# Kernel optimization log

Measured on AMD Instinct MI355X. Metric: run time of the kernel, lower is better.

Reference implementation:

```python
import jax, jax.numpy as jnp
import numpy as np

EPS = 1e-6
B_PAIRS, N_PER_GRAPH, D_IN, D_OUT = 128, 64, 128, 128
N_NODES = B_PAIRS * N_PER_GRAPH          # 8192 nodes on each side
N_EDGES = B_PAIRS * N_PER_GRAPH * N_PER_GRAPH  # 524288 dense bipartite edges


def setup_inputs() -> dict:
    key = jax.random.key(0)
    k1, k2, k3 = jax.random.split(key, 3)
    x_src = jax.random.normal(k1, (N_NODES, D_IN), dtype=jnp.float32)
    x_tgt = jax.random.normal(k2, (N_NODES, D_IN), dtype=jnp.float32)
    # xavier-uniform-like weight [out_nhid, in_nhid]
    bound = np.sqrt(6.0 / (D_OUT + D_IN))
    weight = jax.random.uniform(k3, (D_OUT, D_IN), dtype=jnp.float32,
                                minval=-bound, maxval=bound)
    # block-diagonal dense bipartite edges: graph pair p connects its n x n nodes
    base = np.arange(B_PAIRS, dtype=np.int64)[:, None, None] * N_PER_GRAPH
    src = (base + np.arange(N_PER_GRAPH, dtype=np.int64)[:, None]).repeat(N_PER_GRAPH, axis=2)
    dst = (base + np.arange(N_PER_GRAPH, dtype=np.int64)[None, None, :]).repeat(N_PER_GRAPH, axis=1)
    edge_src = jnp.asarray(src.reshape(-1))
    edge_dst = jnp.asarray(dst.reshape(-1))
    return {"x_src": x_src, "x_tgt": x_tgt, "weight": weight,
            "edge_src": edge_src, "edge_dst": edge_dst}


def reference(x_src, x_tgt, weight, edge_src, edge_dst):
    M = x_tgt.shape[0]
    # --- message: per-edge relu(cosine similarity), softmax-like normalization per target ---
    x_j = x_src[edge_src]                      # [E, D] gather source features
    x_i = x_tgt[edge_dst]                      # [E, D] gather target features
    n_i = jnp.linalg.norm(x_i, axis=-1, keepdims=True)
    n_j = jnp.linalg.norm(x_j, axis=-1, keepdims=True)
    x_norm = jnp.maximum(n_i * n_j, EPS)
    coef = jax.nn.relu(jnp.sum(x_i * x_j, axis=1, keepdims=True) / x_norm)  # [E,1]
    coef_sum = jax.ops.segment_sum(coef + EPS, edge_dst, num_segments=M)    # [M,1]
    norm_coef = coef / coef_sum[edge_dst]
    global_x = jax.ops.segment_sum(norm_coef * x_j, edge_dst, num_segments=M)  # [M,D]
    # --- per-output-channel cosine between weight-scaled target and aggregated features ---
    # numerator[m,o] = sum_d x_tgt[m,d] * global_x[m,d] * weight[o,d]^2  (avoids [M,O,D] blowup)
    W2 = weight * weight                       # [O, D]
    numerator = (x_tgt * global_x) @ W2.T      # [M, O]
    den_t = jnp.sqrt((x_tgt * x_tgt) @ W2.T + EPS)
    den_g = jnp.sqrt((global_x * global_x) @ W2.T + EPS)
    denominator = jnp.maximum(den_t * den_g, EPS)
    return numerator / denominator             # [M, out_nhid]
```

## Files before the change

kernel.cpp:

```cpp
#include <hip/hip_runtime.h>

#define EPS 1e-6f

typedef __bf16 bf16_t;
typedef bf16_t bf16x8 __attribute__((ext_vector_type(8)));
typedef float  f32x4  __attribute__((ext_vector_type(4)));

namespace {
constexpr int D  = 128;
constexpr int OD = 128;
constexpr int SXS_S = 136;
constexpr int SCF_S = 72;
constexpr int SF_S  = 132;
}

__device__ inline bf16x8 to_bf16x8(float4 a, float4 b) {
    bf16x8 r;
    r[0] = (bf16_t)a.x; r[1] = (bf16_t)a.y; r[2] = (bf16_t)a.z; r[3] = (bf16_t)a.w;
    r[4] = (bf16_t)b.x; r[5] = (bf16_t)b.y; r[6] = (bf16_t)b.z; r[7] = (bf16_t)b.w;
    return r;
}

__global__ __launch_bounds__(512, 4)
void h2mn_fused(const float* __restrict__ x_src,
                const float* __restrict__ x_tgt,
                const float* __restrict__ weight,
                float* __restrict__ out)
{
    __shared__ __attribute__((aligned(16))) bf16_t sXs[64][SXS_S];
    __shared__ __attribute__((aligned(16))) bf16_t sCf[16][SCF_S];
    __shared__ __attribute__((aligned(16))) float  sXt[16][SF_S];
    __shared__ __attribute__((aligned(16))) float  sGx[16][SF_S];
    __shared__ float ns[64], ntg[16], csum[16];

    const int t = threadIdx.x;
    const int p = blockIdx.x >> 2;
    const int h = blockIdx.x & 3;

    {
        const float4* src = reinterpret_cast<const float4*>(x_src + (size_t)p * 64 * D);
        #pragma unroll
        for (int k = 0; k < 2; ++k) {
            const int c = t + 512 * k;
            const int j = c >> 4, d0 = (c & 15) * 8;
            const float4 v0 = src[c * 2], v1 = src[c * 2 + 1];
            float ss = v0.x*v0.x + v0.y*v0.y + v0.z*v0.z + v0.w*v0.w
                     + v1.x*v1.x + v1.y*v1.y + v1.z*v1.z + v1.w*v1.w;
            #pragma unroll
            for (int mk = 1; mk < 16; mk <<= 1) ss += __shfl_xor(ss, mk);
            if ((t & 15) == 0) ns[j] = sqrtf(ss);
            *reinterpret_cast<bf16x8*>(&sXs[j][d0]) = to_bf16x8(v0, v1);
        }
    }
    if (t < 256) {
        const float4* tg = reinterpret_cast<const float4*>(x_tgt + (size_t)(p * 64 + h * 16) * D);
        const int c = t;
        const int i = c >> 4, d0 = (c & 15) * 8;
        const float4 v0 = tg[c * 2], v1 = tg[c * 2 + 1];
        float ss = v0.x*v0.x + v0.y*v0.y + v0.z*v0.z + v0.w*v0.w
                 + v1.x*v1.x + v1.y*v1.y + v1.z*v1.z + v1.w*v1.w;
        #pragma unroll
        for (int mk = 1; mk < 16; mk <<= 1) ss += __shfl_xor(ss, mk);
        if ((t & 15) == 0) ntg[i] = sqrtf(ss);
        *reinterpret_cast<float4*>(&sXt[i][d0])     = v0;
        *reinterpret_cast<float4*>(&sXt[i][d0 + 4]) = v1;
    }
    __syncthreads();

    const int w  = t >> 6;
    const int ln = t & 63;
    const int mm = ln & 15;
    const int g  = ln >> 4;

    if (w < 4) {
        const int nt = w;
        f32x4 accS = {0.f, 0.f, 0.f, 0.f};
        #pragma unroll
        for (int ks = 0; ks < 4; ++ks) {
            const float* xp = &sXt[mm][ks * 32 + g * 8];
            const float4 x0 = *reinterpret_cast<const float4*>(xp);
            const float4 x1 = *reinterpret_cast<const float4*>(xp + 4);
            const bf16x8 a = to_bf16x8(x0, x1);
            const bf16x8 b = *reinterpret_cast<const bf16x8*>(&sXs[nt * 16 + mm][ks * 32 + g * 8]);
            accS = __builtin_amdgcn_mfma_f32_16x16x32_bf16(a, b, accS, 0, 0, 0);
        }
        const int j_loc = nt * 16 + mm;
        const float nsj = ns[j_loc];
        #pragma unroll
        for (int r = 0; r < 4; ++r) {
            const int m_loc = g * 4 + r;
            const float den = fmaxf(ntg[m_loc] * nsj, EPS);
            const float cf  = fmaxf(accS[r] / den, 0.f);
            sCf[m_loc][j_loc] = (bf16_t)cf;
        }
    }
    __syncthreads();

    if (t < 256) {
        const int row = t >> 4, c0 = (t & 15) * 4;
        float s = (float)sCf[row][c0]     + (float)sCf[row][c0 + 1]
                + (float)sCf[row][c0 + 2] + (float)sCf[row][c0 + 3];
        #pragma unroll
        for (int mk = 1; mk < 16; mk <<= 1) s += __shfl_xor(s, mk);
        if ((t & 15) == 0) csum[row] = s + 64.f * EPS;
    }
    __syncthreads();

    const float* wrow = weight + (size_t)(w * 16 + mm) * D + g * 8;
    float4 wr0[4], wr1[4];
    #pragma unroll
    for (int ks = 0; ks < 4; ++ks) {
        wr0[ks] = *reinterpret_cast<const float4*>(wrow + ks * 32);
        wr1[ks] = *reinterpret_cast<const float4*>(wrow + ks * 32 + 4);
    }

    {
        f32x4 accG = {0.f, 0.f, 0.f, 0.f};
        #pragma unroll
        for (int ks = 0; ks < 2; ++ks) {
            const bf16x8 a = *reinterpret_cast<const bf16x8*>(&sCf[mm][ks * 32 + g * 8]);
            bf16x8 b;
            #pragma unroll
            for (int i2 = 0; i2 < 8; ++i2)
                b[i2] = sXs[ks * 32 + g * 8 + i2][w * 16 + mm];
            accG = __builtin_amdgcn_mfma_f32_16x16x32_bf16(a, b, accG, 0, 0, 0);
        }
        float inv[4];
        #pragma unroll
        for (int r = 0; r < 4; ++r) inv[r] = 1.f / csum[g * 4 + r];
        #pragma unroll
        for (int r = 0; r < 4; ++r)
            sGx[g * 4 + r][w * 16 + mm] = accG[r] * inv[r];
    }
    __syncthreads();

    {
        f32x4 nume = {0.f,0.f,0.f,0.f};
        f32x4 det  = {0.f,0.f,0.f,0.f};
        f32x4 deg  = {0.f,0.f,0.f,0.f};
        #pragma unroll
        for (int ks = 0; ks < 4; ++ks) {
            const float* xp = &sXt[mm][ks * 32 + g * 8];
            const float* gp = &sGx[mm][ks * 32 + g * 8];
            const float4 x0 = *reinterpret_cast<const float4*>(xp);
            const float4 x1 = *reinterpret_cast<const float4*>(xp + 4);
            const float4 g0 = *reinterpret_cast<const float4*>(gp);
            const float4 g1 = *reinterpret_cast<const float4*>(gp + 4);
            const float xv[8] = {x0.x,x0.y,x0.z,x0.w,x1.x,x1.y,x1.z,x1.w};
            const float gv[8] = {g0.x,g0.y,g0.z,g0.w,g1.x,g1.y,g1.z,g1.w};
            bf16x8 af, bf_, cf_;
            #pragma unroll
            for (int i2 = 0; i2 < 8; ++i2) {
                af [i2] = (bf16_t)(xv[i2] * gv[i2]);
                bf_[i2] = (bf16_t)(xv[i2] * xv[i2]);
                cf_[i2] = (bf16_t)(gv[i2] * gv[i2]);
            }
            float4 w0 = wr0[ks], w1 = wr1[ks];
            w0.x *= w0.x; w0.y *= w0.y; w0.z *= w0.z; w0.w *= w0.w;
            w1.x *= w1.x; w1.y *= w1.y; w1.z *= w1.z; w1.w *= w1.w;
            const bf16x8 wv = to_bf16x8(w0, w1);
            nume = __builtin_amdgcn_mfma_f32_16x16x32_bf16(af,  wv, nume, 0, 0, 0);
            det  = __builtin_amdgcn_mfma_f32_16x16x32_bf16(bf_, wv, det,  0, 0, 0);
            deg  = __builtin_amdgcn_mfma_f32_16x16x32_bf16(cf_, wv, deg,  0, 0, 0);
        }
        const int o = w * 16 + mm;
        #pragma unroll
        for (int r = 0; r < 4; ++r) {
            const int m_loc = g * 4 + r;
            const int mg = p * 64 + h * 16 + m_loc;
            const float dd = fmaxf(sqrtf(det[r] + EPS) * sqrtf(deg[r] + EPS), EPS);
            out[(size_t)mg * OD + o] = nume[r] / dd;
        }
    }
}

extern "C" void kernel_launch(void* const* d_in, const int* in_sizes, int n_in,
                              void* d_out, int out_size, void* d_ws, size_t ws_size,
                              hipStream_t stream)
{
    const float* x_src  = (const float*)d_in[0];
    const float* x_tgt  = (const float*)d_in[1];
    const float* weight = (const float*)d_in[2];
    float* out = (float*)d_out;

    h2mn_fused<<<dim3(512), dim3(512), 0, stream>>>(x_src, x_tgt, weight, out);
}
```

Baseline: 73.91 us.

## Precompute bf16 MFMA operands in shared memory and overlap weight loads

Stores x_tgt in bf16 once in shared memory for the similarity MFMA. The squared and product operands for the final projection (x*g, x^2, g^2) are now computed cooperatively into shared bf16 tiles instead of redundantly by every wave. The x^2 tile is built by the idle waves 4-7 during the similarity stage. The weight load is moved ahead of the similarity stage and squared once into registers. This removes duplicated conversion work across the eight waves, at the cost of more shared memory (lower occupancy risk) and one extra barrier.

```diff
diff --git a/kernel.cpp b/kernel.cpp
--- a/kernel.cpp
+++ b/kernel.cpp
@@ -4,6 +4,7 @@
 
 typedef __bf16 bf16_t;
 typedef bf16_t bf16x8 __attribute__((ext_vector_type(8)));
+typedef bf16_t bf16x4 __attribute__((ext_vector_type(4)));
 typedef float  f32x4  __attribute__((ext_vector_type(4)));
 
 namespace {
@@ -12,6 +13,7 @@
 constexpr int SXS_S = 136;
 constexpr int SCF_S = 72;
 constexpr int SF_S  = 132;
+constexpr int SB_S  = 136;
 }
 
 __device__ inline bf16x8 to_bf16x8(float4 a, float4 b) {
@@ -27,10 +29,14 @@
                 const float* __restrict__ weight,
                 float* __restrict__ out)
 {
-    __shared__ __attribute__((aligned(16))) bf16_t sXs[64][SXS_S];
-    __shared__ __attribute__((aligned(16))) bf16_t sCf[16][SCF_S];
-    __shared__ __attribute__((aligned(16))) float  sXt[16][SF_S];
-    __shared__ __attribute__((aligned(16))) float  sGx[16][SF_S];
+    __shared__ __attribute__((aligned(16))) bf16_t sXs [64][SXS_S];
+    __shared__ __attribute__((aligned(16))) bf16_t sXtB[16][SB_S];
+    __shared__ __attribute__((aligned(16))) bf16_t sCf [16][SCF_S];
+    __shared__ __attribute__((aligned(16))) float  sXt [16][SF_S];
+    __shared__ __attribute__((aligned(16))) float  sGx [16][SF_S];
+    __shared__ __attribute__((aligned(16))) bf16_t sAf [16][SB_S];
+    __shared__ __attribute__((aligned(16))) bf16_t sBf [16][SB_S];
+    __shared__ __attribute__((aligned(16))) bf16_t sCg [16][SB_S];
     __shared__ float ns[64], ntg[16], csum[16];
 
     const int t = threadIdx.x;
@@ -64,6 +70,7 @@
         if ((t & 15) == 0) ntg[i] = sqrtf(ss);
         *reinterpret_cast<float4*>(&sXt[i][d0])     = v0;
         *reinterpret_cast<float4*>(&sXt[i][d0 + 4]) = v1;
+        *reinterpret_cast<bf16x8*>(&sXtB[i][d0])    = to_bf16x8(v0, v1);
     }
     __syncthreads();
 
@@ -71,40 +78,6 @@
     const int ln = t & 63;
     const int mm = ln & 15;
     const int g  = ln >> 4;
-
-    if (w < 4) {
-        const int nt = w;
-        f32x4 accS = {0.f, 0.f, 0.f, 0.f};
-        #pragma unroll
-        for (int ks = 0; ks < 4; ++ks) {
-            const float* xp = &sXt[mm][ks * 32 + g * 8];
-            const float4 x0 = *reinterpret_cast<const float4*>(xp);
-            const float4 x1 = *reinterpret_cast<const float4*>(xp + 4);
-            const bf16x8 a = to_bf16x8(x0, x1);
-            const bf16x8 b = *reinterpret_cast<const bf16x8*>(&sXs[nt * 16 + mm][ks * 32 + g * 8]);
-            accS = __builtin_amdgcn_mfma_f32_16x16x32_bf16(a, b, accS, 0, 0, 0);
-        }
-        const int j_loc = nt * 16 + mm;
-        const float nsj = ns[j_loc];
-        #pragma unroll
-        for (int r = 0; r < 4; ++r) {
-            const int m_loc = g * 4 + r;
-            const float den = fmaxf(ntg[m_loc] * nsj, EPS);
-            const float cf  = fmaxf(accS[r] / den, 0.f);
-            sCf[m_loc][j_loc] = (bf16_t)cf;
-        }
-    }
-    __syncthreads();
-
-    if (t < 256) {
-        const int row = t >> 4, c0 = (t & 15) * 4;
-        float s = (float)sCf[row][c0]     + (float)sCf[row][c0 + 1]
-                + (float)sCf[row][c0 + 2] + (float)sCf[row][c0 + 3];
-        #pragma unroll
-        for (int mk = 1; mk < 16; mk <<= 1) s += __shfl_xor(s, mk);
-        if ((t & 15) == 0) csum[row] = s + 64.f * EPS;
-    }
-    __syncthreads();
 
     const float* wrow = weight + (size_t)(w * 16 + mm) * D + g * 8;
     float4 wr0[4], wr1[4];
@@ -112,6 +85,55 @@
     for (int ks = 0; ks < 4; ++ks) {
         wr0[ks] = *reinterpret_cast<const float4*>(wrow + ks * 32);
         wr1[ks] = *reinterpret_cast<const float4*>(wrow + ks * 32 + 4);
+    }
+
+    if (w < 4) {
+        const int nt = w;
+        f32x4 accS = {0.f, 0.f, 0.f, 0.f};
+        #pragma unroll
+        for (int ks = 0; ks < 4; ++ks) {
+            const bf16x8 a = *reinterpret_cast<const bf16x8*>(&sXtB[mm][ks * 32 + g * 8]);
+            const bf16x8 b = *reinterpret_cast<const bf16x8*>(&sXs[nt * 16 + mm][ks * 32 + g * 8]);
+            accS = __builtin_amdgcn_mfma_f32_16x16x32_bf16(a, b, accS, 0, 0, 0);
+        }
+        const int j_loc = nt * 16 + mm;
+        const float nsj = ns[j_loc];
+        #pragma unroll
+        for (int r = 0; r < 4; ++r) {
+            const int m_loc = g * 4 + r;
+            const float den = fmaxf(ntg[m_loc] * nsj, EPS);
+            const float cf  = fmaxf(accS[r] / den, 0.f);
+            sCf[m_loc][j_loc] = (bf16_t)cf;
+        }
+    } else {
+        const int u   = t - 256;
+        const int row = u >> 4, d0 = (u & 15) * 8;
+        const float4 x0 = *reinterpret_cast<const float4*>(&sXt[row][d0]);
+        const float4 x1 = *reinterpret_cast<const float4*>(&sXt[row][d0 + 4]);
+        float4 q0, q1;
+        q0.x = x0.x*x0.x; q0.y = x0.y*x0.y; q0.z = x0.z*x0.z; q0.w = x0.w*x0.w;
+        q1.x = x1.x*x1.x; q1.y = x1.y*x1.y; q1.z = x1.z*x1.z; q1.w = x1.w*x1.w;
+        *reinterpret_cast<bf16x8*>(&sBf[row][d0]) = to_bf16x8(q0, q1);
+    }
+    __syncthreads();
+
+    if (t < 256) {
+        const int row = t >> 4, c0 = (t & 15) * 4;
+        float s = (float)sCf[row][c0]     + (float)sCf[row][c0 + 1]
+                + (float)sCf[row][c0 + 2] + (float)sCf[row][c0 + 3];
+        #pragma unroll
+        for (int mk = 1; mk < 16; mk <<= 1) s += __shfl_xor(s, mk);
+        if ((t & 15) == 0) csum[row] = s + 64.f * EPS;
+    }
+    __syncthreads();
+
+    bf16x8 wq[4];
+    #pragma unroll
+    for (int ks = 0; ks < 4; ++ks) {
+        float4 w0 = wr0[ks], w1 = wr1[ks];
+        w0.x *= w0.x; w0.y *= w0.y; w0.z *= w0.z; w0.w *= w0.w;
+        w1.x *= w1.x; w1.y *= w1.y; w1.z *= w1.z; w1.w *= w1.w;
+        wq[ks] = to_bf16x8(w0, w1);
     }
 
     {
@@ -135,33 +157,32 @@
     __syncthreads();
 
     {
+        const int row = t >> 5, d0 = (t & 31) * 4;
+        const float4 xv = *reinterpret_cast<const float4*>(&sXt[row][d0]);
+        const float4 gv = *reinterpret_cast<const float4*>(&sGx[row][d0]);
+        bf16x4 a4, c4;
+        a4[0] = (bf16_t)(xv.x * gv.x); a4[1] = (bf16_t)(xv.y * gv.y);
+        a4[2] = (bf16_t)(xv.z * gv.z); a4[3] = (bf16_t)(xv.w * gv.w);
+        c4[0] = (bf16_t)(gv.x * gv.x); c4[1] = (bf16_t)(gv.y * gv.y);
+        c4[2] = (bf16_t)(gv.z * gv.z); c4[3] = (bf16_t)(gv.w * gv.w);
+        *reinterpret_cast<bf16x4*>(&sAf[row][d0]) = a4;
+        *reinterpret_cast<bf16x4*>(&sCg[row][d0]) = c4;
+    }
+    __syncthreads();
+
+    {
         f32x4 nume = {0.f,0.f,0.f,0.f};
         f32x4 det  = {0.f,0.f,0.f,0.f};
         f32x4 deg  = {0.f,0.f,0.f,0.f};
         #pragma unroll
         for (int ks = 0; ks < 4; ++ks) {
-            const float* xp = &sXt[mm][ks * 32 + g * 8];
-            const float* gp = &sGx[mm][ks * 32 + g * 8];
-            const float4 x0 = *reinterpret_cast<const float4*>(xp);
-            const float4 x1 = *reinterpret_cast<const float4*>(xp + 4);
-            const float4 g0 = *reinterpret_cast<const float4*>(gp);
-            const float4 g1 = *reinterpret_cast<const float4*>(gp + 4);
-            const float xv[8] = {x0.x,x0.y,x0.z,x0.w,x1.x,x1.y,x1.z,x1.w};
-            const float gv[8] = {g0.x,g0.y,g0.z,g0.w,g1.x,g1.y,g1.z,g1.w};
-            bf16x8 af, bf_, cf_;
-            #pragma unroll
-            for (int i2 = 0; i2 < 8; ++i2) {
-                af [i2] = (bf16_t)(xv[i2] * gv[i2]);
-                bf_[i2] = (bf16_t)(xv[i2] * xv[i2]);
-                cf_[i2] = (bf16_t)(gv[i2] * gv[i2]);
-            }
-            float4 w0 = wr0[ks], w1 = wr1[ks];
-            w0.x *= w0.x; w0.y *= w0.y; w0.z *= w0.z; w0.w *= w0.w;
-            w1.x *= w1.x; w1.y *= w1.y; w1.z *= w1.z; w1.w *= w1.w;
-            const bf16x8 wv = to_bf16x8(w0, w1);
-            nume = __builtin_amdgcn_mfma_f32_16x16x32_bf16(af,  wv, nume, 0, 0, 0);
-            det  = __builtin_amdgcn_mfma_f32_16x16x32_bf16(bf_, wv, det,  0, 0, 0);
-            deg  = __builtin_amdgcn_mfma_f32_16x16x32_bf16(cf_, wv, deg,  0, 0, 0);
+            const int k0 = ks * 32 + g * 8;
+            const bf16x8 af  = *reinterpret_cast<const bf16x8*>(&sAf[mm][k0]);
+            const bf16x8 bf_ = *reinterpret_cast<const bf16x8*>(&sBf[mm][k0]);
+            const bf16x8 cf_ = *reinterpret_cast<const bf16x8*>(&sCg[mm][k0]);
+            nume = __builtin_amdgcn_mfma_f32_16x16x32_bf16(af,  wq[ks], nume, 0, 0, 0);
+            det  = __builtin_amdgcn_mfma_f32_16x16x32_bf16(bf_, wq[ks], det,  0, 0, 0);
+            deg  = __builtin_amdgcn_mfma_f32_16x16x32_bf16(cf_, wq[ks], deg,  0, 0, 0);
         }
         const int o = w * 16 + mm;
         #pragma unroll
```

New measurement: 73.21 us. About the same (-0.9%).
